# Performance work log

Hardware: AMD Instinct MI355X
Metric: run time of the kernel (lower is better)

The kernel has to match this reference:

```python
import jax, jax.numpy as jnp
import numpy as np
import jax.scipy.linalg

BATCH = 1048576
M_NUM = 2
DT = 0.0166667
NN_RATIO = 0.5
SLOPE = 0.01  # torch LeakyReLU default negative_slope


def setup_inputs() -> dict:
    key = jax.random.key(0)
    ks = jax.random.split(key, 16)
    inp = {}
    inp["SS"] = jax.random.normal(ks[0], (BATCH, 2), dtype=jnp.float32)
    inp["Alphas"] = jax.random.uniform(ks[1], (BATCH, M_NUM), dtype=jnp.float32)
    # per-muscle scalar parameters (positive so sqrt(K*I) is valid)
    inp["K0s"] = jax.random.uniform(ks[2], (M_NUM,), minval=0.5, maxval=1.5)
    inp["K1s"] = jax.random.uniform(ks[3], (M_NUM,), minval=0.5, maxval=1.5)
    inp["L0s"] = jax.random.uniform(ks[4], (M_NUM,), minval=0.5, maxval=1.5)
    inp["L1s"] = jax.random.uniform(ks[5], (M_NUM,), minval=0.1, maxval=0.6)
    inp["Ms"] = jnp.array([1.0, -1.0], dtype=jnp.float32)  # moment arms
    inp["I_p"] = jnp.array([1.0], dtype=jnp.float32)
    inp["B_p"] = jnp.array([0.05], dtype=jnp.float32)
    inp["K_p"] = jnp.array([1.0], dtype=jnp.float32)
    # per-muscle compensational MLP weights: 3-32-32-32-1 (eval mode, dropout off)
    s = 0.1
    inp["W1"] = jax.random.normal(ks[6], (M_NUM, 3, 32)) * s
    inp["b1"] = jax.random.normal(ks[7], (M_NUM, 32)) * s
    inp["W2"] = jax.random.normal(ks[8], (M_NUM, 32, 32)) * s
    inp["b2"] = jax.random.normal(ks[9], (M_NUM, 32)) * s
    inp["W3"] = jax.random.normal(ks[10], (M_NUM, 32, 32)) * s
    inp["b3"] = jax.random.normal(ks[11], (M_NUM, 32)) * s
    inp["W4"] = jax.random.normal(ks[12], (M_NUM, 32, 1)) * s
    inp["b4"] = jax.random.normal(ks[13], (M_NUM, 1)) * s
    return inp


def _leaky(x):
    return jnp.where(x >= 0, x, SLOPE * x)


def reference(SS, Alphas, K0s, K1s, L0s, L1s, Ms, I_p, B_p, K_p,
              W1, b1, W2, b2, W3, b3, W4, b4):
    B = SS.shape[0]
    a = jnp.clip(Alphas, 0.0, 1.0)                      # (B, m)
    # muscle length / speed via scalar moment arms
    l = SS[:, 0:1] * Ms[None, :]                        # (B, m)
    dl = SS[:, 1:2] * Ms[None, :]                       # (B, m)
    # compensational MLPs, vectorized over muscles
    x = jnp.stack([l, dl, a], axis=-1)                  # (B, m, 3)
    h = _leaky(jnp.einsum('bmi,mio->bmo', x, W1) + b1[None])
    h = _leaky(jnp.einsum('bmi,mio->bmo', h, W2) + b2[None])
    h = _leaky(jnp.einsum('bmi,mio->bmo', h, W3) + b3[None])
    nn_out = jnp.tanh(jnp.einsum('bmi,mio->bmo', h, W4) + b4[None])[..., 0] * NN_RATIO  # (B, m)

    I0, B0p, K0p = I_p[0], B_p[0], K_p[0]
    K_m = K0s[None, :] + K1s[None, :] * a               # (B, m)
    K_tot = jnp.sum(K_m * Ms[None, :] ** 2, axis=1)     # (B,)
    A10 = -(K_tot + K0p) / I0
    D = 2.0 * jnp.sqrt(K_tot * I0)
    A11 = -(D + B0p) / I0
    B_F = K_m * (L0s[None, :] + L1s[None, :] * a - jnp.abs(l)) \
        + K1s[None, :] * L1s[None, :] * a * a * nn_out   # (B, m)
    B10 = jnp.sum(B_F * Ms[None, :], axis=1) / I0       # (B,)

    # Build block matrix M6 = [[A*dt, B*dt, 0], [0, 0, I2], [0, 0, 0]]
    M6 = jnp.zeros((B, 6, 6), dtype=SS.dtype)
    M6 = M6.at[:, 0, 1].set(DT)
    M6 = M6.at[:, 1, 0].set(A10 * DT)
    M6 = M6.at[:, 1, 1].set(A11 * DT)
    M6 = M6.at[:, 1, 2].set(B10 * DT)
    M6 = M6.at[:, 1, 3].set(DT / I0)
    M6 = M6.at[:, 2, 4].set(1.0)
    M6 = M6.at[:, 3, 5].set(1.0)

    expMT = jax.vmap(jax.scipy.linalg.expm)(M6)         # (B, 6, 6)
    Ad = expMT[:, :2, :2]
    Bd1 = expMT[:, :2, 4:6]
    Bd0 = expMT[:, :2, 2:4] - Bd1
    u = jnp.array([1.0, 0.0], dtype=SS.dtype)           # U0 = U1 = [1, 0]
    SSout = (jnp.einsum('bij,bj->bi', Ad, SS)
             + jnp.einsum('bij,j->bi', Bd0, u)
             + jnp.einsum('bij,j->bi', Bd1, u))          # (B, 2)
    return SSout[:, :1], SSout
```

## Files before the change

kernel.cpp:

```cpp
#include <hip/hip_runtime.h>
#include <hip/hip_bf16.h>

#define NTHREADS 256
#define WAVES    4
#define GPW      2
#define DT_F     0.0166667f

typedef _Float16 f16x4 __attribute__((ext_vector_type(4)));
typedef _Float16 f16x2 __attribute__((ext_vector_type(2)));
typedef float    f32x4 __attribute__((ext_vector_type(4)));

#define BF16_PROBE 0xBF803F80u

#define OW1 0
#define OB1 192
#define OW2 256
#define OB2 2304
#define OW3 2368
#define OB3 4416
#define OW4 4480
#define OB4 4544
#define SMEM_F 4560

__device__ __forceinline__ float leaky(float x) { return fmaxf(x, 0.01f * x); }

__device__ __forceinline__ float tanh_fast(float x) {
    const float xc = fminf(fmaxf(x, -10.0f), 10.0f);
    const float t  = __expf(2.0f * xc);
    return (t - 1.0f) * __builtin_amdgcn_rcpf(t + 1.0f);
}

__device__ __forceinline__ f16x2 pkrtz(float a, float b) {
    return __builtin_bit_cast(f16x2, __builtin_amdgcn_cvt_pkrtz(a, b));
}

__device__ __forceinline__ f16x4 leaky_cvt(const f32x4 D) {
    f16x2 lo = pkrtz(D[0], D[1]);
    f16x2 hi = pkrtz(D[2], D[3]);
    const f16x2 sl = {(_Float16)0.01f, (_Float16)0.01f};
    lo = __builtin_elementwise_max(lo, lo * sl);
    hi = __builtin_elementwise_max(hi, hi * sl);
    return __builtin_shufflevector(lo, hi, 0, 1, 2, 3);
}

__device__ __forceinline__ void epilogue_math(
    const float* P, float ss0, float ss1, float a0, float a1,
    float nn0, float nn1, float& o0f, float& o1f)
{
    const float K00 = P[0], K01 = P[1], K10 = P[2], K11 = P[3];
    const float L00 = P[4], L01 = P[5], L10 = P[6], L11 = P[7];
    const float Ms0 = P[8], Ms1 = P[9];
    const float I0  = P[10], B0p = P[11], K0p = P[12];

    const float Km0   = fmaf(K10, a0, K00);
    const float Km1   = fmaf(K11, a1, K01);
    const float K_tot = Km0*Ms0*Ms0 + Km1*Ms1*Ms1;
    const float invI  = 1.0f / I0;
    const float A10   = -(K_tot + K0p) * invI;
    const float Dd    = 2.0f * sqrtf(K_tot * I0);
    const float A11   = -(Dd + B0p) * invI;
    const float absl0 = fabsf(ss0 * Ms0);
    const float absl1 = fabsf(ss0 * Ms1);
    const float BF0   = Km0 * (L00 + L10*a0 - absl0) + K10*L10*a0*a0*nn0;
    const float BF1   = Km1 * (L01 + L11*a1 - absl1) + K11*L11*a1*a1*nn1;
    const float B10   = (BF0*Ms0 + BF1*Ms1) * invI;

    const float t01 = DT_F;
    const float t10 = A10 * DT_F;
    const float t11 = A11 * DT_F;

    float p00 = 1.0f/5040.0f, p01 = 0.0f, p10 = 0.0f, p11 = 1.0f/5040.0f;
    const float coef[6] = {1.0f/720.0f, 1.0f/120.0f, 1.0f/24.0f,
                           1.0f/6.0f,   0.5f,        1.0f};
    #pragma unroll
    for (int j = 0; j < 6; ++j) {
        const float cj  = coef[j];
        const float n00 = p01*t10 + cj;
        const float n01 = p00*t01 + p01*t11;
        const float n10 = p11*t10;
        const float n11 = p10*t01 + p11*t11 + cj;
        p00 = n00; p01 = n01; p10 = n10; p11 = n11;
    }
    const float e00 = 1.0f + t01*p10;
    const float e01 = t01*p11;
    const float e10 = t10*p00 + t11*p10;
    const float e11 = 1.0f + t10*p01 + t11*p11;

    const float cscale = DT_F * B10;
    o0f = fmaf(e00, ss0, fmaf(e01, ss1, p01 * cscale));
    o1f = fmaf(e10, ss0, fmaf(e11, ss1, p11 * cscale));
}

__device__ __forceinline__ float ldb(const __hip_bfloat16* p, int i) {
    return __bfloat162float(p[i]);
}

__device__ void run_bf16_fallback(
    const void* SSv, const void* ALv, const void* K0sv, const void* K1sv,
    const void* L0sv, const void* L1sv, const void* Msv, const void* I_pv,
    const void* B_pv, const void* K_pv, const void* W1v, const void* b1v,
    const void* W2v, const void* b2v, const void* W3v, const void* b3v,
    const void* W4v, const void* b4v, void* outv, int batch)
{
    const __hip_bfloat16* SS = (const __hip_bfloat16*)SSv;
    const __hip_bfloat16* AL = (const __hip_bfloat16*)ALv;
    const __hip_bfloat16* W1 = (const __hip_bfloat16*)W1v;
    const __hip_bfloat16* b1 = (const __hip_bfloat16*)b1v;
    const __hip_bfloat16* W2 = (const __hip_bfloat16*)W2v;
    const __hip_bfloat16* b2 = (const __hip_bfloat16*)b2v;
    const __hip_bfloat16* W3 = (const __hip_bfloat16*)W3v;
    const __hip_bfloat16* b3 = (const __hip_bfloat16*)b3v;
    const __hip_bfloat16* W4 = (const __hip_bfloat16*)W4v;
    const __hip_bfloat16* b4 = (const __hip_bfloat16*)b4v;

    float P[13];
    P[0] = ldb((const __hip_bfloat16*)K0sv, 0); P[1] = ldb((const __hip_bfloat16*)K0sv, 1);
    P[2] = ldb((const __hip_bfloat16*)K1sv, 0); P[3] = ldb((const __hip_bfloat16*)K1sv, 1);
    P[4] = ldb((const __hip_bfloat16*)L0sv, 0); P[5] = ldb((const __hip_bfloat16*)L0sv, 1);
    P[6] = ldb((const __hip_bfloat16*)L1sv, 0); P[7] = ldb((const __hip_bfloat16*)L1sv, 1);
    P[8] = ldb((const __hip_bfloat16*)Msv, 0);  P[9] = ldb((const __hip_bfloat16*)Msv, 1);
    P[10] = ldb((const __hip_bfloat16*)I_pv, 0);
    P[11] = ldb((const __hip_bfloat16*)B_pv, 0);
    P[12] = ldb((const __hip_bfloat16*)K_pv, 0);

    const int stride = gridDim.x * blockDim.x;
    for (int e = blockIdx.x * blockDim.x + threadIdx.x; e < batch; e += stride) {
        const float ss0 = ldb(SS, 2*e), ss1 = ldb(SS, 2*e+1);
        float a0 = fminf(fmaxf(ldb(AL, 2*e),   0.0f), 1.0f);
        float a1 = fminf(fmaxf(ldb(AL, 2*e+1), 0.0f), 1.0f);
        float nn[2];
        #pragma unroll 1
        for (int m = 0; m < 2; ++m) {
            const float am = m ? a1 : a0;
            const float l = ss0 * P[8+m], dl = ss1 * P[8+m];
            float h[32];
            #pragma unroll
            for (int o = 0; o < 32; ++o)
                h[o] = leaky(fmaf(l, ldb(W1, m*96+o),
                             fmaf(dl, ldb(W1, m*96+32+o),
                             fmaf(am, ldb(W1, m*96+64+o), ldb(b1, m*32+o)))));
            float g[32];
            #pragma unroll 1
            for (int oc = 0; oc < 4; ++oc) {
                float acc[8];
                #pragma unroll
                for (int j = 0; j < 8; ++j) acc[j] = ldb(b2, m*32+oc*8+j);
                #pragma unroll
                for (int k = 0; k < 32; ++k) {
                    #pragma unroll
                    for (int j = 0; j < 8; ++j)
                        acc[j] = fmaf(h[k], ldb(W2, m*1024+k*32+oc*8+j), acc[j]);
                }
                #pragma unroll
                for (int j = 0; j < 8; ++j) g[oc*8+j] = leaky(acc[j]);
            }
            float h3[32];
            #pragma unroll 1
            for (int oc = 0; oc < 4; ++oc) {
                float acc[8];
                #pragma unroll
                for (int j = 0; j < 8; ++j) acc[j] = ldb(b3, m*32+oc*8+j);
                #pragma unroll
                for (int k = 0; k < 32; ++k) {
                    #pragma unroll
                    for (int j = 0; j < 8; ++j)
                        acc[j] = fmaf(g[k], ldb(W3, m*1024+k*32+oc*8+j), acc[j]);
                }
                #pragma unroll
                for (int j = 0; j < 8; ++j) h3[oc*8+j] = leaky(acc[j]);
            }
            float acc = ldb(b4, m);
            #pragma unroll
            for (int k = 0; k < 32; ++k) acc = fmaf(h3[k], ldb(W4, m*32+k), acc);
            nn[m] = tanh_fast(acc) * 0.5f;
        }
        float o0f, o1f;
        epilogue_math(P, ss0, ss1, a0, a1, nn[0], nn[1], o0f, o1f);
        __hip_bfloat16* out0 = (__hip_bfloat16*)outv;
        __hip_bfloat162* out1 = (__hip_bfloat162*)(out0 + batch);
        out0[e] = __float2bfloat16(o0f);
        __hip_bfloat162 pr;
        pr.x = __float2bfloat16(o0f);
        pr.y = __float2bfloat16(o1f);
        out1[e] = pr;
    }
}

__global__ __launch_bounds__(NTHREADS) void joint_kernel(
    const void* __restrict__ SSv, const void* __restrict__ ALv,
    const void* __restrict__ K0sv, const void* __restrict__ K1sv,
    const void* __restrict__ L0sv, const void* __restrict__ L1sv,
    const void* __restrict__ Msv,  const void* __restrict__ I_pv,
    const void* __restrict__ B_pv, const void* __restrict__ K_pv,
    const void* __restrict__ W1v,  const void* __restrict__ b1v,
    const void* __restrict__ W2v,  const void* __restrict__ b2v,
    const void* __restrict__ W3v,  const void* __restrict__ b3v,
    const void* __restrict__ W4v,  const void* __restrict__ b4v,
    void* __restrict__ outv, int batch)
{
    const unsigned probe = *(const unsigned*)Msv;
    if (probe == BF16_PROBE) {
        run_bf16_fallback(SSv, ALv, K0sv, K1sv, L0sv, L1sv, Msv, I_pv, B_pv,
                          K_pv, W1v, b1v, W2v, b2v, W3v, b3v, W4v, b4v,
                          outv, batch);
        return;
    }

    const float* SS = (const float*)SSv;
    const float* AL = (const float*)ALv;
    const float* W1 = (const float*)W1v;  const float* b1 = (const float*)b1v;
    const float* W2 = (const float*)W2v;  const float* b2 = (const float*)b2v;
    const float* W3 = (const float*)W3v;  const float* b3 = (const float*)b3v;
    const float* W4 = (const float*)W4v;  const float* b4 = (const float*)b4v;

    const int tid  = threadIdx.x;
    const int wave = tid >> 6;
    const int lane = tid & 63;
    const int n    = lane & 15;
    const int q    = lane >> 4;

    __shared__ __align__(16) float sm[SMEM_F];
    for (int i = tid; i < 192;  i += NTHREADS) sm[OW1+i] = W1[i];
    for (int i = tid; i < 2048; i += NTHREADS) { sm[OW2+i] = W2[i]; sm[OW3+i] = W3[i]; }
    for (int i = tid; i < 64;   i += NTHREADS) {
        sm[OB1+i] = b1[i]; sm[OB2+i] = b2[i];
        sm[OB3+i] = b3[i]; sm[OW4+i] = W4[i];
    }
    if (tid < 2) sm[OB4+tid] = b4[tid];
    __syncthreads();

    f16x4 A1[2][2];
    #pragma unroll
    for (int mi = 0; mi < 2; ++mi)
        #pragma unroll
        for (int i = 0; i < 2; ++i)
            #pragma unroll
            for (int j = 0; j < 4; ++j) {
                const int k = q*4 + j;
                float v = 0.0f;
                if (k < 3)       v = sm[OW1 + mi*96 + k*32 + i*16 + n];
                else if (k == 3) v = sm[OB1 + mi*32 + i*16 + n];
                A1[mi][i][j] = (_Float16)v;
            }
    f16x4 A2[2][2][2], A3[2][2][2];
    #pragma unroll
    for (int mi = 0; mi < 2; ++mi)
        #pragma unroll
        for (int i = 0; i < 2; ++i)
            #pragma unroll
            for (int kb = 0; kb < 2; ++kb)
                #pragma unroll
                for (int j = 0; j < 4; ++j) {
                    const int in = kb*16 + q*4 + j;
                    A2[mi][i][kb][j] = (_Float16)sm[OW2 + mi*1024 + in*32 + i*16 + n];
                    A3[mi][i][kb][j] = (_Float16)sm[OW3 + mi*1024 + in*32 + i*16 + n];
                }
    f16x4 A4[2][2];
    #pragma unroll
    for (int mi = 0; mi < 2; ++mi)
        #pragma unroll
        for (int kb = 0; kb < 2; ++kb)
            #pragma unroll
            for (int j = 0; j < 4; ++j)
                A4[mi][kb][j] = (_Float16)sm[OW4 + mi*32 + kb*16 + q*4 + j];
    f32x4 Cb2[2][2], Cb3[2][2];
    #pragma unroll
    for (int mi = 0; mi < 2; ++mi) {
        #pragma unroll
        for (int i = 0; i < 2; ++i) {
            Cb2[mi][i] = *(const f32x4*)&sm[OB2 + mi*32 + i*16 + q*4];
            Cb3[mi][i] = *(const f32x4*)&sm[OB3 + mi*32 + i*16 + q*4];
        }
    }
    const float b4s0 = sm[OB4], b4s1 = sm[OB4+1];

    float P[13];
    P[0]  = ((const float*)K0sv)[0]; P[1]  = ((const float*)K0sv)[1];
    P[2]  = ((const float*)K1sv)[0]; P[3]  = ((const float*)K1sv)[1];
    P[4]  = ((const float*)L0sv)[0]; P[5]  = ((const float*)L0sv)[1];
    P[6]  = ((const float*)L1sv)[0]; P[7]  = ((const float*)L1sv)[1];
    P[8]  = ((const float*)Msv)[0];  P[9]  = ((const float*)Msv)[1];
    P[10] = ((const float*)I_pv)[0];
    P[11] = ((const float*)B_pv)[0];
    P[12] = ((const float*)K_pv)[0];

    const f32x4 zero = {0.0f, 0.0f, 0.0f, 0.0f};
    const int groupBase = (blockIdx.x * WAVES + wave) * GPW;

    #pragma unroll 1
    for (int g = 0; g < GPW; ++g) {
        const int ebase = (groupBase + g) * 64;
        float my_r0 = 0.0f, my_r1 = 0.0f;

        #pragma unroll
        for (int t = 0; t < 4; ++t) {
            const int e  = ebase + t*16 + n;
            const int eg = min(e, batch - 1);
            const float2 s  = ((const float2*)SS)[eg];
            const float2 al = ((const float2*)AL)[eg];
            const float a0 = fminf(fmaxf(al.x, 0.0f), 1.0f);
            const float a1 = fminf(fmaxf(al.y, 0.0f), 1.0f);

            float rr[2];
            #pragma unroll
            for (int mi = 0; mi < 2; ++mi) {
                const float Msm = P[8 + mi];
                const float am  = mi ? a1 : a0;
                const f16x2 blo = pkrtz(s.x * Msm, s.y * Msm);
                const f16x2 bhi = pkrtz(am, 1.0f);
                const f16x4 B1 = __builtin_shufflevector(blo, bhi, 0, 1, 2, 3);

                f32x4 D0 = __builtin_amdgcn_mfma_f32_16x16x16f16(A1[mi][0], B1, zero, 0, 0, 0);
                f32x4 D1 = __builtin_amdgcn_mfma_f32_16x16x16f16(A1[mi][1], B1, zero, 0, 0, 0);
                const f16x4 B2_0 = leaky_cvt(D0);
                const f16x4 B2_1 = leaky_cvt(D1);

                f32x4 E0 = __builtin_amdgcn_mfma_f32_16x16x16f16(A2[mi][0][1], B2_1,
                           __builtin_amdgcn_mfma_f32_16x16x16f16(A2[mi][0][0], B2_0,
                               Cb2[mi][0], 0, 0, 0), 0, 0, 0);
                f32x4 E1 = __builtin_amdgcn_mfma_f32_16x16x16f16(A2[mi][1][1], B2_1,
                           __builtin_amdgcn_mfma_f32_16x16x16f16(A2[mi][1][0], B2_0,
                               Cb2[mi][1], 0, 0, 0), 0, 0, 0);
                const f16x4 B3_0 = leaky_cvt(E0);
                const f16x4 B3_1 = leaky_cvt(E1);

                f32x4 F0 = __builtin_amdgcn_mfma_f32_16x16x16f16(A3[mi][0][1], B3_1,
                           __builtin_amdgcn_mfma_f32_16x16x16f16(A3[mi][0][0], B3_0,
                               Cb3[mi][0], 0, 0, 0), 0, 0, 0);
                f32x4 F1 = __builtin_amdgcn_mfma_f32_16x16x16f16(A3[mi][1][1], B3_1,
                           __builtin_amdgcn_mfma_f32_16x16x16f16(A3[mi][1][0], B3_0,
                               Cb3[mi][1], 0, 0, 0), 0, 0, 0);
                const f16x4 B4_0 = leaky_cvt(F0);
                const f16x4 B4_1 = leaky_cvt(F1);

                f32x4 G = __builtin_amdgcn_mfma_f32_16x16x16f16(A4[mi][1], B4_1,
                          __builtin_amdgcn_mfma_f32_16x16x16f16(A4[mi][0], B4_0,
                              zero, 0, 0, 0), 0, 0, 0);
                rr[mi] = G[0] + (mi ? b4s1 : b4s0);
            }

            const bool own = (q == t);
            my_r0 = own ? rr[0] : my_r0;
            my_r1 = own ? rr[1] : my_r1;
        }

        const int eo  = ebase + lane;
        const int eog = min(eo, batch - 1);
        const float2 s  = ((const float2*)SS)[eog];
        const float2 al = ((const float2*)AL)[eog];
        const float a0 = fminf(fmaxf(al.x, 0.0f), 1.0f);
        const float a1 = fminf(fmaxf(al.y, 0.0f), 1.0f);
        const float nn0 = tanh_fast(my_r0) * 0.5f;
        const float nn1 = tanh_fast(my_r1) * 0.5f;
        float o0f, o1f;
        epilogue_math(P, s.x, s.y, a0, a1, nn0, nn1, o0f, o1f);
        if (eo < batch) {
            ((float*)outv)[eo] = o0f;
            ((float2*)((float*)outv + batch))[eo] = make_float2(o0f, o1f);
        }
    }
}

extern "C" void kernel_launch(void* const* d_in, const int* in_sizes, int n_in,
                              void* d_out, int out_size, void* d_ws, size_t ws_size,
                              hipStream_t stream) {
    const int batch = in_sizes[0] / 2;
    const int elemsPerBlock = 64 * GPW * WAVES;
    const int grid = (batch + elemsPerBlock - 1) / elemsPerBlock;
    joint_kernel<<<grid, NTHREADS, 0, stream>>>(
        d_in[0], d_in[1], d_in[2], d_in[3], d_in[4], d_in[5], d_in[6],
        d_in[7], d_in[8], d_in[9], d_in[10], d_in[11], d_in[12], d_in[13],
        d_in[14], d_in[15], d_in[16], d_in[17], d_out, batch);
}
```

Baseline: 131.9 us.

## Interleave two MLP tiles per layer to hide MFMA latency; double groups per wave

The MLP loop over four 16-element tiles becomes two passes, each handling two tiles, with every layer's MFMAs issued for both tiles and both muscles before the leaky conversions. This gives more independent MFMA chains to cover dependent-issue latency. GPW also goes from 2 to 4, halving the grid so each block's weight-fragment setup covers more groups, at the cost of fewer blocks and more live registers, which may lower occupancy.

```diff
diff --git a/kernel.cpp b/kernel.cpp
--- a/kernel.cpp
+++ b/kernel.cpp
@@ -3,7 +3,7 @@
 
 #define NTHREADS 256
 #define WAVES    4
-#define GPW      2
+#define GPW      4
 #define DT_F     0.0166667f
 
 typedef _Float16 f16x4 __attribute__((ext_vector_type(4)));
@@ -292,68 +292,114 @@
         const int ebase = (groupBase + g) * 64;
         float my_r0 = 0.0f, my_r1 = 0.0f;
 
-        #pragma unroll
-        for (int t = 0; t < 4; ++t) {
-            const int e  = ebase + t*16 + n;
-            const int eg = min(e, batch - 1);
-            const float2 s  = ((const float2*)SS)[eg];
-            const float2 al = ((const float2*)AL)[eg];
-            const float a0 = fminf(fmaxf(al.x, 0.0f), 1.0f);
-            const float a1 = fminf(fmaxf(al.y, 0.0f), 1.0f);
-
-            float rr[2];
-            #pragma unroll
-            for (int mi = 0; mi < 2; ++mi) {
-                const float Msm = P[8 + mi];
-                const float am  = mi ? a1 : a0;
-                const f16x2 blo = pkrtz(s.x * Msm, s.y * Msm);
-                const f16x2 bhi = pkrtz(am, 1.0f);
-                const f16x4 B1 = __builtin_shufflevector(blo, bhi, 0, 1, 2, 3);
-
-                f32x4 D0 = __builtin_amdgcn_mfma_f32_16x16x16f16(A1[mi][0], B1, zero, 0, 0, 0);
-                f32x4 D1 = __builtin_amdgcn_mfma_f32_16x16x16f16(A1[mi][1], B1, zero, 0, 0, 0);
-                const f16x4 B2_0 = leaky_cvt(D0);
-                const f16x4 B2_1 = leaky_cvt(D1);
-
-                f32x4 E0 = __builtin_amdgcn_mfma_f32_16x16x16f16(A2[mi][0][1], B2_1,
-                           __builtin_amdgcn_mfma_f32_16x16x16f16(A2[mi][0][0], B2_0,
-                               Cb2[mi][0], 0, 0, 0), 0, 0, 0);
-                f32x4 E1 = __builtin_amdgcn_mfma_f32_16x16x16f16(A2[mi][1][1], B2_1,
-                           __builtin_amdgcn_mfma_f32_16x16x16f16(A2[mi][1][0], B2_0,
-                               Cb2[mi][1], 0, 0, 0), 0, 0, 0);
-                const f16x4 B3_0 = leaky_cvt(E0);
-                const f16x4 B3_1 = leaky_cvt(E1);
-
-                f32x4 F0 = __builtin_amdgcn_mfma_f32_16x16x16f16(A3[mi][0][1], B3_1,
-                           __builtin_amdgcn_mfma_f32_16x16x16f16(A3[mi][0][0], B3_0,
-                               Cb3[mi][0], 0, 0, 0), 0, 0, 0);
-                f32x4 F1 = __builtin_amdgcn_mfma_f32_16x16x16f16(A3[mi][1][1], B3_1,
-                           __builtin_amdgcn_mfma_f32_16x16x16f16(A3[mi][1][0], B3_0,
-                               Cb3[mi][1], 0, 0, 0), 0, 0, 0);
-                const f16x4 B4_0 = leaky_cvt(F0);
-                const f16x4 B4_1 = leaky_cvt(F1);
-
-                f32x4 G = __builtin_amdgcn_mfma_f32_16x16x16f16(A4[mi][1], B4_1,
-                          __builtin_amdgcn_mfma_f32_16x16x16f16(A4[mi][0], B4_0,
-                              zero, 0, 0, 0), 0, 0, 0);
-                rr[mi] = G[0] + (mi ? b4s1 : b4s0);
+        #pragma unroll 1
+        for (int p = 0; p < 2; ++p) {
+            const int t0 = 2*p, t1 = 2*p + 1;
+
+            float2 s[2], al[2];
+            float a0c[2], a1c[2];
+            #pragma unroll
+            for (int ti = 0; ti < 2; ++ti) {
+                const int e  = ebase + (2*p + ti)*16 + n;
+                const int eg = min(e, batch - 1);
+                s[ti]  = ((const float2*)SS)[eg];
+                al[ti] = ((const float2*)AL)[eg];
+                a0c[ti] = fminf(fmaxf(al[ti].x, 0.0f), 1.0f);
+                a1c[ti] = fminf(fmaxf(al[ti].y, 0.0f), 1.0f);
             }
 
-            const bool own = (q == t);
-            my_r0 = own ? rr[0] : my_r0;
-            my_r1 = own ? rr[1] : my_r1;
+            f16x4 B1[2][2];
+            #pragma unroll
+            for (int ti = 0; ti < 2; ++ti)
+                #pragma unroll
+                for (int mi = 0; mi < 2; ++mi) {
+                    const float Msm = P[8 + mi];
+                    const float am  = mi ? a1c[ti] : a0c[ti];
+                    const f16x2 blo = pkrtz(s[ti].x * Msm, s[ti].y * Msm);
+                    const f16x2 bhi = pkrtz(am, 1.0f);
+                    B1[ti][mi] = __builtin_shufflevector(blo, bhi, 0, 1, 2, 3);
+                }
+
+            f32x4 D[2][2][2];
+            #pragma unroll
+            for (int ti = 0; ti < 2; ++ti)
+                #pragma unroll
+                for (int mi = 0; mi < 2; ++mi) {
+                    D[ti][mi][0] = __builtin_amdgcn_mfma_f32_16x16x16f16(A1[mi][0], B1[ti][mi], zero, 0, 0, 0);
+                    D[ti][mi][1] = __builtin_amdgcn_mfma_f32_16x16x16f16(A1[mi][1], B1[ti][mi], zero, 0, 0, 0);
+                }
+            f16x4 Bx[2][2][2];
+            #pragma unroll
+            for (int ti = 0; ti < 2; ++ti)
+                #pragma unroll
+                for (int mi = 0; mi < 2; ++mi) {
+                    Bx[ti][mi][0] = leaky_cvt(D[ti][mi][0]);
+                    Bx[ti][mi][1] = leaky_cvt(D[ti][mi][1]);
+                }
+
+            #pragma unroll
+            for (int ti = 0; ti < 2; ++ti)
+                #pragma unroll
+                for (int mi = 0; mi < 2; ++mi) {
+                    D[ti][mi][0] = __builtin_amdgcn_mfma_f32_16x16x16f16(A2[mi][0][1], Bx[ti][mi][1],
+                                   __builtin_amdgcn_mfma_f32_16x16x16f16(A2[mi][0][0], Bx[ti][mi][0],
+                                       Cb2[mi][0], 0, 0, 0), 0, 0, 0);
+                    D[ti][mi][1] = __builtin_amdgcn_mfma_f32_16x16x16f16(A2[mi][1][1], Bx[ti][mi][1],
+                                   __builtin_amdgcn_mfma_f32_16x16x16f16(A2[mi][1][0], Bx[ti][mi][0],
+                                       Cb2[mi][1], 0, 0, 0), 0, 0, 0);
+                }
+            #pragma unroll
+            for (int ti = 0; ti < 2; ++ti)
+                #pragma unroll
+                for (int mi = 0; mi < 2; ++mi) {
+                    Bx[ti][mi][0] = leaky_cvt(D[ti][mi][0]);
+                    Bx[ti][mi][1] = leaky_cvt(D[ti][mi][1]);
+                }
+
+            #pragma unroll
+            for (int ti = 0; ti < 2; ++ti)
+                #pragma unroll
+                for (int mi = 0; mi < 2; ++mi) {
+                    D[ti][mi][0] = __builtin_amdgcn_mfma_f32_16x16x16f16(A3[mi][0][1], Bx[ti][mi][1],
+                                   __builtin_amdgcn_mfma_f32_16x16x16f16(A3[mi][0][0], Bx[ti][mi][0],
+                                       Cb3[mi][0], 0, 0, 0), 0, 0, 0);
+                    D[ti][mi][1] = __builtin_amdgcn_mfma_f32_16x16x16f16(A3[mi][1][1], Bx[ti][mi][1],
+                                   __builtin_amdgcn_mfma_f32_16x16x16f16(A3[mi][1][0], Bx[ti][mi][0],
+                                       Cb3[mi][1], 0, 0, 0), 0, 0, 0);
+                }
+            #pragma unroll
+            for (int ti = 0; ti < 2; ++ti)
+                #pragma unroll
+                for (int mi = 0; mi < 2; ++mi) {
+                    Bx[ti][mi][0] = leaky_cvt(D[ti][mi][0]);
+                    Bx[ti][mi][1] = leaky_cvt(D[ti][mi][1]);
+                }
+
+            #pragma unroll
+            for (int ti = 0; ti < 2; ++ti) {
+                const bool own = (q == (2*p + ti));
+                #pragma unroll
+                for (int mi = 0; mi < 2; ++mi) {
+                    f32x4 G = __builtin_amdgcn_mfma_f32_16x16x16f16(A4[mi][1], Bx[ti][mi][1],
+                              __builtin_amdgcn_mfma_f32_16x16x16f16(A4[mi][0], Bx[ti][mi][0],
+                                  zero, 0, 0, 0), 0, 0, 0);
+                    const float r = G[0] + (mi ? b4s1 : b4s0);
+                    if (mi == 0) my_r0 = own ? r : my_r0;
+                    else         my_r1 = own ? r : my_r1;
+                }
+            }
         }
 
         const int eo  = ebase + lane;
         const int eog = min(eo, batch - 1);
-        const float2 s  = ((const float2*)SS)[eog];
-        const float2 al = ((const float2*)AL)[eog];
-        const float a0 = fminf(fmaxf(al.x, 0.0f), 1.0f);
-        const float a1 = fminf(fmaxf(al.y, 0.0f), 1.0f);
+        const float2 se  = ((const float2*)SS)[eog];
+        const float2 ale = ((const float2*)AL)[eog];
+        const float a0 = fminf(fmaxf(ale.x, 0.0f), 1.0f);
+        const float a1 = fminf(fmaxf(ale.y, 0.0f), 1.0f);
         const float nn0 = tanh_fast(my_r0) * 0.5f;
         const float nn1 = tanh_fast(my_r1) * 0.5f;
         float o0f, o1f;
-        epilogue_math(P, s.x, s.y, a0, a1, nn0, nn1, o0f, o1f);
+        epilogue_math(P, se.x, se.y, a0, a1, nn0, nn1, o0f, o1f);
         if (eo < batch) {
             ((float*)outv)[eo] = o0f;
             ((float2*)((float*)outv + batch))[eo] = make_float2(o0f, o1f);
```

Result: faster. 129.2 us (-2.0%).
